# Optimization experiments

Hardware: AMD Instinct MI355X
Metric: run time of the kernel (lower is better)

Reference implementation:

```python
import jax, jax.numpy as jnp
import numpy as np

PENALTY_FACTOR = 2.0
THRESHOLD = 0.01


def setup_inputs() -> dict:
    key = jax.random.key(0)
    k1, k2 = jax.random.split(key)
    B, N = 256, 65536
    prediction = jax.random.normal(k1, (B, N), dtype=jnp.float32)
    label = jax.random.normal(k2, (B, N), dtype=jnp.float32)
    return {"prediction": prediction, "label": label}


def _first_last_significant(mask, half):
    # mask: [B, half] bool. Returns per-row first/last True index,
    # defaulting to (0, half-1) when the row has no True entries
    # (matching the torch fallback branch).
    any_m = jnp.any(mask, axis=1)
    first = jnp.argmax(mask, axis=1)                      # 0 if all False
    last = (half - 1) - jnp.argmax(mask[:, ::-1], axis=1)  # half-1 if all False
    first = jnp.where(any_m, first, 0)
    last = jnp.where(any_m, last, half - 1)
    return first, last


def reference(prediction, label):
    B, N = label.shape
    half = N // 2
    label_real, label_imag = label[:, :half], label[:, half:]
    pred_real, pred_imag = prediction[:, :half], prediction[:, half:]

    label_phase = jnp.arctan2(label_imag, label_real)
    pred_phase = jnp.arctan2(pred_imag, pred_real)
    label_int = label_real ** 2 + label_imag ** 2
    pred_int = pred_real ** 2 + pred_imag ** 2

    fr, lr = _first_last_significant(jnp.abs(label_real) > THRESHOLD, half)
    fi, li = _first_last_significant(jnp.abs(label_imag) > THRESHOLD, half)

    idx = jnp.arange(half)[None, :]  # [1, half]
    w_real = jnp.where((idx < fr[:, None]) | (idx > lr[:, None]), PENALTY_FACTOR, 1.0)
    w_imag = jnp.where((idx < fi[:, None]) | (idx > li[:, None]), PENALTY_FACTOR, 1.0)

    mse_real = w_real * (pred_real - label_real) ** 2
    mse_imag = w_imag * (pred_imag - label_imag) ** 2
    mse_int = (pred_int - label_int) ** 2
    mse_phase = (pred_phase - label_phase) ** 2

    per_sample = (mse_real.mean(axis=1) + mse_imag.mean(axis=1)
                  + 50.0 * mse_int.mean(axis=1) + 0.0 * mse_phase.mean(axis=1))
    return per_sample.mean()
```

## Files before the change

kernel.cpp:

```cpp
#include <hip/hip_runtime.h>

constexpr int HALF  = 32768;
constexpr int NSEG  = 8;
constexpr int SEG   = HALF / NSEG;
constexpr int TPB   = 256;
constexpr int NPASS = SEG / 4 / TPB;
constexpr float THRESH = 0.01f;


__global__ __launch_bounds__(TPB)
void seg_kernel(const float* __restrict__ pred, const float* __restrict__ label,
                float* __restrict__ ws)
{
    const int seg = blockIdx.x;
    const int row = blockIdx.y;
    const int t    = threadIdx.x;
    const int wave = t >> 6, lane = t & 63;

    const size_t row4 = (size_t)row * (size_t)(2 * HALF / 4);
    const float4* lr4 = (const float4*)label + row4 + (size_t)seg * (SEG / 4);
    const float4* li4 = lr4 + (HALF / 4);
    const float4* pr4 = (const float4*)pred + row4 + (size_t)seg * (SEG / 4);
    const float4* pi4 = pr4 + (HALF / 4);

    __shared__ float s_m[NPASS][4][9];

    #pragma unroll
    for (int p = 0; p < NPASS; ++p) {
        const int g = p * TPB + t;
        float4 a = lr4[g], b = li4[g], pp = pr4[g], q = pi4[g];

        float rs = 0.f, rp = 0.f, rq = 0.f; int rh = 0;
        float is = 0.f, ip = 0.f, iq = 0.f; int ih = 0;
        float ds = 0.f;
#define STEP(ax, bx, px, qx)                                          \
        {                                                             \
            float dr = (px) - (ax), di = (qx) - (bx);                 \
            float cr = dr * dr, ci = di * di;                         \
            float lint = (ax) * (ax) + (bx) * (bx);                   \
            float pint = (px) * (px) + (qx) * (qx);                   \
            float dd = pint - lint; ds += dd * dd;                    \
            rs += cr; is += ci;                                       \
            if (fabsf(ax) > THRESH) { rh = 1; rq = 0.f; }             \
            else { rq += cr; if (!rh) rp += cr; }                     \
            if (fabsf(bx) > THRESH) { ih = 1; iq = 0.f; }             \
            else { iq += ci; if (!ih) ip += ci; }                     \
        }
        STEP(a.x, b.x, pp.x, q.x) STEP(a.y, b.y, pp.y, q.y)
        STEP(a.z, b.z, pp.z, q.z) STEP(a.w, b.w, pp.w, q.w)
#undef STEP

        #pragma unroll
        for (int off = 1; off < 64; off <<= 1) {
            float Rrs = __shfl_down(rs, off), Rrp = __shfl_down(rp, off), Rrq = __shfl_down(rq, off);
            int   Rrh = __shfl_down(rh, off);
            float Ris = __shfl_down(is, off), Rip = __shfl_down(ip, off), Riq = __shfl_down(iq, off);
            int   Rih = __shfl_down(ih, off);
            float Rds = __shfl_down(ds, off);
            rp = rh ? rp : (rs + Rrp);
            rq = Rrh ? Rrq : (rq + Rrs);
            rs += Rrs; rh |= Rrh;
            ip = ih ? ip : (is + Rip);
            iq = Rih ? Riq : (iq + Ris);
            is += Ris; ih |= Rih;
            ds += Rds;
        }
        if (lane == 0) {
            float* d = s_m[p][wave];
            d[0] = rs; d[1] = rp; d[2] = rq; d[3] = (float)rh;
            d[4] = is; d[5] = ip; d[6] = iq; d[7] = (float)ih;
            d[8] = ds;
        }
    }
    __syncthreads();

    if (t == 0) {
        float rs = 0.f, rp = 0.f, rq = 0.f, rh = 0.f;
        float is = 0.f, ip = 0.f, iq = 0.f, ih = 0.f;
        float ds = 0.f;
        for (int p = 0; p < NPASS; ++p)
            for (int w = 0; w < 4; ++w) {
                const float* d = s_m[p][w];
                float Rrs = d[0], Rrp = d[1], Rrq = d[2], Rrh = d[3];
                float Ris = d[4], Rip = d[5], Riq = d[6], Rih = d[7];
                rp = (rh != 0.f) ? rp : (rs + Rrp);
                rq = (Rrh != 0.f) ? Rrq : (rq + Rrs);
                rs += Rrs; rh += Rrh;
                ip = (ih != 0.f) ? ip : (is + Rip);
                iq = (Rih != 0.f) ? Riq : (iq + Ris);
                is += Ris; ih += Rih;
                ds += d[8];
            }
        float4* o4 = (float4*)(ws + ((size_t)row * NSEG + seg) * 12);
        o4[0] = make_float4(rs, rp, rq, rh);
        o4[1] = make_float4(is, ip, iq, ih);
        o4[2] = make_float4(ds, 0.f, 0.f, 0.f);
    }
}

__global__ void finalize_kernel(const float* __restrict__ ws,
                                float* __restrict__ out, int rows)
{
    const int t = threadIdx.x;
    float total = 0.f;
    for (int r = t; r < rows; r += 256) {
        float rs = 0.f, rp = 0.f, rq = 0.f, rh = 0.f;
        float is = 0.f, ip = 0.f, iq = 0.f, ih = 0.f;
        float ds = 0.f;
        const float4* o4 = (const float4*)(ws + (size_t)r * NSEG * 12);
        for (int s = 0; s < NSEG; ++s) {
            float4 A = o4[s * 3 + 0], B = o4[s * 3 + 1], C = o4[s * 3 + 2];
            rp = (rh != 0.f) ? rp : (rs + A.y);
            rq = (A.w != 0.f) ? A.z : (rq + A.x);
            rs += A.x; rh += A.w;
            ip = (ih != 0.f) ? ip : (is + B.y);
            iq = (B.w != 0.f) ? B.z : (iq + B.x);
            is += B.x; ih += B.w;
            ds += C.x;
        }
        float extra_r = (rh != 0.f) ? (rp + rq) : 0.f;
        float extra_i = (ih != 0.f) ? (ip + iq) : 0.f;
        total += rs + is + 50.f * ds + extra_r + extra_i;
    }
    #pragma unroll
    for (int off = 32; off > 0; off >>= 1) total += __shfl_down(total, off);
    __shared__ float s[4];
    if ((t & 63) == 0) s[t >> 6] = total;
    __syncthreads();
    if (t == 0) out[0] = (s[0] + s[1] + s[2] + s[3]) * (1.0f / ((float)HALF * (float)rows));
}

extern "C" void kernel_launch(void* const* d_in, const int* in_sizes, int n_in,
                              void* d_out, int out_size, void* d_ws, size_t ws_size,
                              hipStream_t stream) {
    const float* pred  = (const float*)d_in[0];
    const float* label = (const float*)d_in[1];
    float* out = (float*)d_out;
    float* ws  = (float*)d_ws;

    const int rows = in_sizes[0] / (2 * HALF);

    dim3 grid(NSEG, rows);
    seg_kernel<<<grid, TPB, 0, stream>>>(pred, label, ws);
    finalize_kernel<<<1, 256, 0, stream>>>(ws, out, rows);
}
```

Before: 34.92 us.

## Process 16 contiguous elements per thread and reduce once per block

Each thread now loads four consecutive float4s from each of the four streams (16 contiguous elements) and runs the first/last-significant scan serially over them. The block then does one wave-shuffle reduction, where before it did one per pass. This cuts the reduction and shared-memory overhead per element. NSEG grows from 8 to 8 (SEG 4096), and each thread's strided float4 loads give less coalesced access. The branches in the scan are replaced by selects.

```diff
diff --git a/kernel.cpp b/kernel.cpp
--- a/kernel.cpp
+++ b/kernel.cpp
@@ -1,10 +1,10 @@
 #include <hip/hip_runtime.h>
 
-constexpr int HALF  = 32768;
-constexpr int NSEG  = 8;
-constexpr int SEG   = HALF / NSEG;
-constexpr int TPB   = 256;
-constexpr int NPASS = SEG / 4 / TPB;
+constexpr int HALF = 32768;
+constexpr int TPB  = 256;
+constexpr int CPT  = 16;
+constexpr int SEG  = TPB * CPT;
+constexpr int NSEG = HALF / SEG;
 constexpr float THRESH = 0.01f;
 
 
@@ -17,84 +17,98 @@
     const int t    = threadIdx.x;
     const int wave = t >> 6, lane = t & 63;
 
-    const size_t row4 = (size_t)row * (size_t)(2 * HALF / 4);
-    const float4* lr4 = (const float4*)label + row4 + (size_t)seg * (SEG / 4);
+    const size_t base4 = (size_t)row * (size_t)(2 * HALF / 4)
+                       + (size_t)seg * (SEG / 4) + (size_t)t * 4;
+    const float4* lr4 = (const float4*)label + base4;
     const float4* li4 = lr4 + (HALF / 4);
-    const float4* pr4 = (const float4*)pred + row4 + (size_t)seg * (SEG / 4);
+    const float4* pr4 = (const float4*)pred + base4;
     const float4* pi4 = pr4 + (HALF / 4);
 
-    __shared__ float s_m[NPASS][4][9];
+    float4 A[4], Bv[4], P[4], Q[4];
+    #pragma unroll
+    for (int j = 0; j < 4; ++j) { A[j] = lr4[j]; }
+    #pragma unroll
+    for (int j = 0; j < 4; ++j) { Bv[j] = li4[j]; }
+    #pragma unroll
+    for (int j = 0; j < 4; ++j) { P[j] = pr4[j]; }
+    #pragma unroll
+    for (int j = 0; j < 4; ++j) { Q[j] = pi4[j]; }
+
+    float rs = 0.f, rp = 0.f, rq = 0.f; int rh = 0;
+    float is = 0.f, ip = 0.f, iq = 0.f; int ih = 0;
+    float ds = 0.f;
+
+#define STEP(ax, bx, px, qx)                                   \
+    {                                                          \
+        float dr = (px) - (ax), di = (qx) - (bx);              \
+        float cr = dr * dr, ci = di * di;                      \
+        float lint = (ax) * (ax) + (bx) * (bx);                \
+        float pint = (px) * (px) + (qx) * (qx);                \
+        float dd = pint - lint; ds += dd * dd;                 \
+        rs += cr; is += ci;                                    \
+        bool sr = fabsf(ax) > THRESH;                          \
+        bool si = fabsf(bx) > THRESH;                          \
+        rq = sr ? 0.f : (rq + cr);                             \
+        rp = (sr || rh) ? rp : (rp + cr);                      \
+        rh |= (int)sr;                                         \
+        iq = si ? 0.f : (iq + ci);                             \
+        ip = (si || ih) ? ip : (ip + ci);                      \
+        ih |= (int)si;                                         \
+    }
 
     #pragma unroll
-    for (int p = 0; p < NPASS; ++p) {
-        const int g = p * TPB + t;
-        float4 a = lr4[g], b = li4[g], pp = pr4[g], q = pi4[g];
-
-        float rs = 0.f, rp = 0.f, rq = 0.f; int rh = 0;
-        float is = 0.f, ip = 0.f, iq = 0.f; int ih = 0;
-        float ds = 0.f;
-#define STEP(ax, bx, px, qx)                                          \
-        {                                                             \
-            float dr = (px) - (ax), di = (qx) - (bx);                 \
-            float cr = dr * dr, ci = di * di;                         \
-            float lint = (ax) * (ax) + (bx) * (bx);                   \
-            float pint = (px) * (px) + (qx) * (qx);                   \
-            float dd = pint - lint; ds += dd * dd;                    \
-            rs += cr; is += ci;                                       \
-            if (fabsf(ax) > THRESH) { rh = 1; rq = 0.f; }             \
-            else { rq += cr; if (!rh) rp += cr; }                     \
-            if (fabsf(bx) > THRESH) { ih = 1; iq = 0.f; }             \
-            else { iq += ci; if (!ih) ip += ci; }                     \
-        }
-        STEP(a.x, b.x, pp.x, q.x) STEP(a.y, b.y, pp.y, q.y)
-        STEP(a.z, b.z, pp.z, q.z) STEP(a.w, b.w, pp.w, q.w)
+    for (int j = 0; j < 4; ++j) {
+        STEP(A[j].x, Bv[j].x, P[j].x, Q[j].x)
+        STEP(A[j].y, Bv[j].y, P[j].y, Q[j].y)
+        STEP(A[j].z, Bv[j].z, P[j].z, Q[j].z)
+        STEP(A[j].w, Bv[j].w, P[j].w, Q[j].w)
+    }
 #undef STEP
 
-        #pragma unroll
-        for (int off = 1; off < 64; off <<= 1) {
-            float Rrs = __shfl_down(rs, off), Rrp = __shfl_down(rp, off), Rrq = __shfl_down(rq, off);
-            int   Rrh = __shfl_down(rh, off);
-            float Ris = __shfl_down(is, off), Rip = __shfl_down(ip, off), Riq = __shfl_down(iq, off);
-            int   Rih = __shfl_down(ih, off);
-            float Rds = __shfl_down(ds, off);
-            rp = rh ? rp : (rs + Rrp);
-            rq = Rrh ? Rrq : (rq + Rrs);
-            rs += Rrs; rh |= Rrh;
-            ip = ih ? ip : (is + Rip);
-            iq = Rih ? Riq : (iq + Ris);
-            is += Ris; ih |= Rih;
-            ds += Rds;
-        }
-        if (lane == 0) {
-            float* d = s_m[p][wave];
-            d[0] = rs; d[1] = rp; d[2] = rq; d[3] = (float)rh;
-            d[4] = is; d[5] = ip; d[6] = iq; d[7] = (float)ih;
-            d[8] = ds;
-        }
+    #pragma unroll
+    for (int off = 1; off < 64; off <<= 1) {
+        float Rrs = __shfl_down(rs, off), Rrp = __shfl_down(rp, off), Rrq = __shfl_down(rq, off);
+        int   Rrh = __shfl_down(rh, off);
+        float Ris = __shfl_down(is, off), Rip = __shfl_down(ip, off), Riq = __shfl_down(iq, off);
+        int   Rih = __shfl_down(ih, off);
+        float Rds = __shfl_down(ds, off);
+        rp = rh ? rp : (rs + Rrp);
+        rq = Rrh ? Rrq : (rq + Rrs);
+        rs += Rrs; rh |= Rrh;
+        ip = ih ? ip : (is + Rip);
+        iq = Rih ? Riq : (iq + Ris);
+        is += Ris; ih |= Rih;
+        ds += Rds;
+    }
+
+    __shared__ float s_m[4][9];
+    if (lane == 0) {
+        float* d = s_m[wave];
+        d[0] = rs; d[1] = rp; d[2] = rq; d[3] = (float)rh;
+        d[4] = is; d[5] = ip; d[6] = iq; d[7] = (float)ih;
+        d[8] = ds;
     }
     __syncthreads();
 
     if (t == 0) {
-        float rs = 0.f, rp = 0.f, rq = 0.f, rh = 0.f;
-        float is = 0.f, ip = 0.f, iq = 0.f, ih = 0.f;
-        float ds = 0.f;
-        for (int p = 0; p < NPASS; ++p)
-            for (int w = 0; w < 4; ++w) {
-                const float* d = s_m[p][w];
-                float Rrs = d[0], Rrp = d[1], Rrq = d[2], Rrh = d[3];
-                float Ris = d[4], Rip = d[5], Riq = d[6], Rih = d[7];
-                rp = (rh != 0.f) ? rp : (rs + Rrp);
-                rq = (Rrh != 0.f) ? Rrq : (rq + Rrs);
-                rs += Rrs; rh += Rrh;
-                ip = (ih != 0.f) ? ip : (is + Rip);
-                iq = (Rih != 0.f) ? Riq : (iq + Ris);
-                is += Ris; ih += Rih;
-                ds += d[8];
-            }
+        float ars = 0.f, arp = 0.f, arq = 0.f, arh = 0.f;
+        float ais = 0.f, aip = 0.f, aiq = 0.f, aih = 0.f;
+        float ads = 0.f;
+        #pragma unroll
+        for (int w = 0; w < 4; ++w) {
+            const float* d = s_m[w];
+            arp = (arh != 0.f) ? arp : (ars + d[1]);
+            arq = (d[3] != 0.f) ? d[2] : (arq + d[0]);
+            ars += d[0]; arh += d[3];
+            aip = (aih != 0.f) ? aip : (ais + d[5]);
+            aiq = (d[7] != 0.f) ? d[6] : (aiq + d[4]);
+            ais += d[4]; aih += d[7];
+            ads += d[8];
+        }
         float4* o4 = (float4*)(ws + ((size_t)row * NSEG + seg) * 12);
-        o4[0] = make_float4(rs, rp, rq, rh);
-        o4[1] = make_float4(is, ip, iq, ih);
-        o4[2] = make_float4(ds, 0.f, 0.f, 0.f);
+        o4[0] = make_float4(ars, arp, arq, arh);
+        o4[1] = make_float4(ais, aip, aiq, aih);
+        o4[2] = make_float4(ads, 0.f, 0.f, 0.f);
     }
 }
 
```

Measured after the change: 31.52 us. -9.7%, faster.
